# Performance work log

Hardware: AMD Instinct MI355X
Metric: run time of the kernel (lower is better)

The kernel has to match this reference:

```python
import jax, jax.numpy as jnp
import numpy as np

B, N, C = 64, 8192, 64
C4 = C // 4
EPS_BN = 1e-5


def setup_inputs() -> dict:
    key = jax.random.key(0)
    ks = jax.random.split(key, 12)
    s = 0.05
    return {
        "x": jax.random.normal(ks[0], (B, N, 10), jnp.float32),
        "y": jax.random.normal(ks[1], (B, N, 13), jnp.float32),
        "W_l": jax.random.normal(ks[2], (10, C), jnp.float32) * s,
        "b_l": jax.random.normal(ks[3], (C,), jnp.float32) * s,
        "W_r": jax.random.normal(ks[4], (13, C), jnp.float32) * s,
        "b_r": jax.random.normal(ks[5], (C,), jnp.float32) * s,
        "W_qk": jax.random.normal(ks[6], (C4, C), jnp.float32) * s,  # shared q/k 1x1-conv weight
        "W_v": jax.random.normal(ks[7], (C, C), jnp.float32) * s,
        "b_v": jax.random.normal(ks[8], (C,), jnp.float32) * s,
        "W_t": jax.random.normal(ks[9], (C, C), jnp.float32) * s,
        "b_t": jax.random.normal(ks[10], (C,), jnp.float32) * s,
        "gamma": jnp.ones((C,), jnp.float32),
        "beta": jnp.zeros((C,), jnp.float32),
    }


def reference(x, y, W_l, b_l, W_r, b_r, W_qk, W_v, b_v, W_t, b_t, gamma, beta):
    # x: [B,N,10] -> linear_l; y: [B,N,13] -> linear_r  (torch keeps [B,C,N]; we keep [B,N,C])
    X = x @ W_l + b_l                                   # [B,N,C]
    Y = y @ W_r + b_r                                   # [B,N,C]
    # 1x1 convs == per-point matmuls; attention runs ACROSS the batch dim per point n
    xq = jnp.einsum('bnc,dc->nbd', X, W_qk)             # [N,B,C/4]
    yk = jnp.einsum('bnc,dc->nbd', Y, W_qk)             # [N,B,C/4] (shared weight)
    yv = jnp.einsum('bnc,dc->nbd', Y, W_v) + b_v        # [N,B,C]
    energy = jnp.einsum('nbd,ned->nbe', xq, yk)         # [N,B,B]
    attn = jax.nn.softmax(energy, axis=-1)
    # extra L1 renormalization over dim=1 (offset-attention style)
    attn = attn / (1e-9 + attn.sum(axis=1, keepdims=True))
    yr = jnp.einsum('nbe,nec->bnc', attn, yv)           # [B,N,C]
    # trans_conv -> BatchNorm (training-mode batch stats) -> ReLU -> residual -> max over points
    t = jnp.einsum('bnc,dc->bnd', X - yr, W_t) + b_t    # [B,N,C]
    mean = t.mean(axis=(0, 1))
    var = t.var(axis=(0, 1))                            # biased var, as BN uses
    tn = gamma * (t - mean) * jax.lax.rsqrt(var + EPS_BN) + beta
    xres = X + jax.nn.relu(tn)                          # [B,N,C]
    return jnp.max(xres, axis=1)[:, :, None]            # [B,C,1] to match torch layout
```

## Files before the change

### kernel.cpp

```cpp
#include <hip/hip_runtime.h>

#define B_ 64
#define N_ 8192

using short8 = __attribute__((ext_vector_type(8))) short;
using f32x4  = __attribute__((ext_vector_type(4))) float;

#define MFMA16(a, b, c) __builtin_amdgcn_mfma_f32_16x16x32_bf16((a), (b), (c), 0, 0, 0)

__device__ inline unsigned short f2bf(float f) {
  union { float f; unsigned int u; } v; v.f = f;
  return (unsigned short)((v.u + 0x8000u) >> 16);
}
__device__ inline float bf2f(unsigned int hi16_in_low) {
  union { unsigned int u; float f; } v; v.u = hi16_in_low << 16;
  return v.f;
}


__global__ void k0_prep(const float* __restrict__ W_l, const float* __restrict__ b_l,
                        const float* __restrict__ W_r, const float* __restrict__ b_r,
                        const float* __restrict__ W_qk, const float* __restrict__ W_v,
                        const float* __restrict__ b_v, const float* __restrict__ W_t,
                        float* __restrict__ wsf) {
  const int tid = threadIdx.x;
  unsigned short* wb   = (unsigned short*)(wsf + 66688);
  unsigned short* BM   = wb;
  unsigned short* BL   = wb + 512;
  unsigned short* BRV2 = wb + 2560;
  unsigned short* BT   = wb + 4608;
  if (blockIdx.x == 0) {
    __shared__ float Wlq[11 * 16], Wrk[14 * 16];
    for (int idx = tid; idx < 11 * 16; idx += 256) {
      int i = idx >> 4, d = idx & 15;
      const float* a = (i < 10) ? (W_l + i * 64) : b_l;
      float s = 0.f;
      for (int c = 0; c < 64; ++c) s = fmaf(a[c], W_qk[d * 64 + c], s);
      Wlq[idx] = s;
    }
    for (int idx = tid; idx < 14 * 16; idx += 256) {
      int j = idx >> 4, d = idx & 15;
      const float* a = (j < 13) ? (W_r + j * 64) : b_r;
      float s = 0.f;
      for (int c = 0; c < 64; ++c) s = fmaf(a[c], W_qk[d * 64 + c], s);
      Wrk[idx] = s;
    }
    __syncthreads();
    for (int idx = tid; idx < 512; idx += 256) {
      int j = idx >> 5, kk = idx & 31;
      unsigned short o = 0;
      if (j < 14 && kk < 11) {
        float s = 0.f;
        for (int d = 0; d < 16; ++d) s = fmaf(Wlq[kk * 16 + d], Wrk[j * 16 + d], s);
        o = f2bf(s);
      }
      BM[idx] = o;
    }
  } else if (blockIdx.x == 1) {
    for (int idx = tid; idx < 2048; idx += 256) {
      int c = idx >> 5, kk = idx & 31;
      unsigned short o = 0;
      if (kk < 13) {
        float s = 0.f;
        for (int j = 0; j < 64; ++j) s = fmaf(W_r[kk * 64 + j], W_v[c * 64 + j], s);
        o = f2bf(s);
      } else if (kk == 13) {
        float s = b_v[c];
        for (int j = 0; j < 64; ++j) s = fmaf(b_r[j], W_v[c * 64 + j], s);
        o = f2bf(s);
      }
      BRV2[idx] = o;
    }
  } else if (blockIdx.x == 2) {
    for (int idx = tid; idx < 2048; idx += 256) {
      int c = idx >> 5, kk = idx & 31;
      unsigned short o = 0;
      if (kk < 10) o = f2bf(W_l[kk * 64 + c]);
      else if (kk == 10) o = f2bf(b_l[c]);
      BL[idx] = o;
    }
    for (int i = tid; i < 1024; i += 256) wsf[i] = 0.f;
  } else {
    for (int i = tid; i < 4096; i += 256) BT[i] = f2bf(W_t[i]);
  }
}

__global__ __launch_bounds__(256, 6)
void k1_attn(const float* __restrict__ x, const float* __restrict__ y,
             const float* __restrict__ wsf, const float* __restrict__ b_t,
             float* __restrict__ stats) {
  __shared__ __align__(16) short Axy[64 * 40];
  __shared__ __align__(16) short YT[16 * 72];
  __shared__ __align__(16) short awZ[4 * 1152];
  __shared__ __align__(16) short GU[4 * 256];
  __shared__ float scr[512];

  const unsigned short* wb   = (const unsigned short*)(wsf + 66688);
  const unsigned short* BM   = wb;
  const unsigned short* BL   = wb + 512;
  const unsigned short* BRV2 = wb + 2560;
  const unsigned short* BT   = wb + 4608;
  unsigned short* tg = (unsigned short*)(wsf + 66688) + 8704;

  const int n    = blockIdx.x;
  const int tid  = threadIdx.x;
  const int w    = tid >> 6;
  const int lane = tid & 63;
  const int l15  = lane & 15;
  const int q    = lane >> 4;
  const int r0   = w * 16;
  short* const aw = awZ + w * 1152;
  short* const gu = GU + w * 256;

  {
    const int b = tid >> 2, i = tid & 3;
    const float* xp = x + ((size_t)b * N_ + n) * 10;
    const float* yp = y + ((size_t)b * N_ + n) * 13;
    short* Ar = Axy + b * 40;
    Ar[i]     = (short)f2bf(xp[i]);
    Ar[i + 4] = (short)f2bf(xp[i + 4]);
    short v8 = 0;
    if (i < 2) v8 = (short)f2bf(xp[i + 8]);
    else if (i == 2) v8 = (short)0x3F80;
    Ar[i + 8]  = v8;
    Ar[i + 12] = 0;
    const short y0 = (short)f2bf(yp[i]);
    const short y1 = (short)f2bf(yp[i + 4]);
    const short y2 = (short)f2bf(yp[i + 8]);
    short y3 = 0;
    if (i == 0) y3 = (short)f2bf(yp[12]);
    else if (i == 1) y3 = (short)0x3F80;
    Ar[16 + i] = y0;  Ar[20 + i] = y1;  Ar[24 + i] = y2;  Ar[28 + i] = y3;
    YT[i * 72 + b] = y0;  YT[(i + 4) * 72 + b] = y1;
    YT[(i + 8) * 72 + b] = y2;  YT[(i + 12) * 72 + b] = y3;
  }
  __syncthreads();

  const short8 z8 = {0, 0, 0, 0, 0, 0, 0, 0};
  const f32x4 zero4 = {0.f, 0.f, 0.f, 0.f};
  const short8 aA = *(const short8*)&Axy[(r0 + l15) * 40 + q * 8];

  f32x4 G = MFMA16(aA, *(const short8*)&BM[l15 * 32 + q * 8], zero4);
  f32x4 X[4];
#pragma unroll
  for (int f = 0; f < 4; ++f)
    X[f] = MFMA16(aA, *(const short8*)&BL[(f * 16 + l15) * 32 + q * 8], zero4);
#pragma unroll
  for (int j = 0; j < 4; ++j) gu[(q * 4 + j) * 16 + l15] = (short)f2bf(G[j]);

  short8 aG = z8;
  if (q < 2) aG = *(const short8*)&gu[l15 * 16 + q * 8];
  f32x4 E[4];
#pragma unroll
  for (int f = 0; f < 4; ++f) {
    short8 bk = z8;
    if (q < 2) bk = *(const short8*)&Axy[(f * 16 + l15) * 40 + 16 + q * 8];
    E[f] = MFMA16(aG, bk, zero4);
  }

  float inv_r[4];
#pragma unroll
  for (int j = 0; j < 4; ++j) {
    float s = 0.f;
#pragma unroll
    for (int f = 0; f < 4; ++f) { E[f][j] = __expf(E[f][j]); s += E[f][j]; }
    s += __shfl_xor(s, 1);
    s += __shfl_xor(s, 2);
    s += __shfl_xor(s, 4);
    s += __shfl_xor(s, 8);
    inv_r[j] = 1.0f / s;
  }
#pragma unroll
  for (int f = 0; f < 4; ++f) {
    float cs = E[f][0] * inv_r[0] + E[f][1] * inv_r[1] + E[f][2] * inv_r[2] + E[f][3] * inv_r[3];
    cs += __shfl_xor(cs, 16);
    cs += __shfl_xor(cs, 32);
    if (lane < 16) scr[w * 64 + f * 16 + l15] = cs;
  }
  __syncthreads();
  float csvv[4];
#pragma unroll
  for (int f = 0; f < 4; ++f) {
    const int col = f * 16 + l15;
    csvv[f] = 1.0f / (1e-9f + scr[col] + scr[64 + col] + scr[128 + col] + scr[192 + col]);
  }
#pragma unroll
  for (int f = 0; f < 4; ++f)
#pragma unroll
    for (int j = 0; j < 4; ++j)
      aw[(q * 4 + j) * 72 + f * 16 + l15] = (short)f2bf(E[f][j] * inv_r[j] * csvv[f]);

  const short8 aA0 = *(const short8*)&aw[l15 * 72 + q * 8];
  const short8 aA1 = *(const short8*)&aw[l15 * 72 + 32 + q * 8];

  f32x4 U = MFMA16(aA0, *(const short8*)&YT[l15 * 72 + q * 8], zero4);
  U = MFMA16(aA1, *(const short8*)&YT[l15 * 72 + 32 + q * 8], U);
#pragma unroll
  for (int j = 0; j < 4; ++j) gu[(q * 4 + j) * 16 + l15] = (short)f2bf(U[j]);
  short8 aU = z8;
  if (q < 2) aU = *(const short8*)&gu[l15 * 16 + q * 8];

#pragma unroll
  for (int f = 0; f < 4; ++f) {
    f32x4 yr = MFMA16(aU, *(const short8*)&BRV2[(f * 16 + l15) * 32 + q * 8], zero4);
#pragma unroll
    for (int j = 0; j < 4; ++j)
      aw[(q * 4 + j) * 72 + f * 16 + l15] = (short)f2bf(X[f][j] - yr[j]);
  }

  const short8 aZ0 = *(const short8*)&aw[l15 * 72 + q * 8];
  const short8 aZ1 = *(const short8*)&aw[l15 * 72 + 32 + q * 8];
  f32x4 t[4];
#pragma unroll
  for (int f = 0; f < 4; ++f) {
    const int c = f * 16 + l15;
    const float bT = b_t[c];
    t[f] = MFMA16(aZ0, *(const short8*)&BT[c * 64 + q * 8], ((f32x4){bT, bT, bT, bT}));
    t[f] = MFMA16(aZ1, *(const short8*)&BT[c * 64 + 32 + q * 8], t[f]);
#pragma unroll
    for (int j = 0; j < 4; ++j)
      tg[(size_t)(r0 + q * 4 + j) * (N_ * 64) + (size_t)n * 64 + c] = f2bf(t[f][j]);
  }
  __syncthreads();
#pragma unroll
  for (int f = 0; f < 4; ++f) {
    float s = 0.f, ss = 0.f;
#pragma unroll
    for (int j = 0; j < 4; ++j) { s += t[f][j]; ss = fmaf(t[f][j], t[f][j], ss); }
    s  += __shfl_xor(s, 16);  s  += __shfl_xor(s, 32);
    ss += __shfl_xor(ss, 16); ss += __shfl_xor(ss, 32);
    if (lane < 16) {
      scr[w * 64 + f * 16 + l15]       = s;
      scr[256 + w * 64 + f * 16 + l15] = ss;
    }
  }
  __syncthreads();
  if (tid < 64) {
    const float s  = scr[tid] + scr[64 + tid] + scr[128 + tid] + scr[192 + tid];
    const float ss = scr[256 + tid] + scr[320 + tid] + scr[384 + tid] + scr[448 + tid];
    float* st = stats + (n & 7) * 128;
    atomicAdd(&st[tid], s);
    atomicAdd(&st[64 + tid], ss);
  }
}

__global__ void k2_stats(const float* __restrict__ stats, float* __restrict__ meanr) {
  const int c = threadIdx.x;
  if (c < 64) {
    float s = 0.f, ss = 0.f;
    for (int r = 0; r < 8; ++r) { s += stats[r * 128 + c]; ss += stats[r * 128 + 64 + c]; }
    const float inv = 1.0f / (float)(B_ * N_);
    const float mu = s * inv;
    const float var = fmaf(ss, inv, -mu * mu);
    meanr[c] = mu;
    meanr[64 + c] = rsqrtf(var + 1e-5f);
  }
}

__global__ __launch_bounds__(256)
void k3_max(const float* __restrict__ x, const float* __restrict__ W_l,
            const float* __restrict__ b_l, const float* __restrict__ gamma,
            const float* __restrict__ beta, const unsigned short* __restrict__ tg,
            const float* __restrict__ meanr, float* __restrict__ pmax)
{
  const int b = blockIdx.x >> 4;
  const int chunk = blockIdx.x & 15;
  const int wv = threadIdx.x >> 6;
  const int lane = threadIdx.x & 63;
  const int c0 = (lane & 15) * 4;
  const int nsub = lane >> 4;
  float4 wl4[10];
#pragma unroll
  for (int k = 0; k < 10; ++k) wl4[k] = *(const float4*)&W_l[k * 64 + c0];
  const float4 bl  = *(const float4*)&b_l[c0];
  const float4 g   = *(const float4*)&gamma[c0];
  const float4 be  = *(const float4*)&beta[c0];
  const float4 mu  = *(const float4*)&meanr[c0];
  const float4 rs  = *(const float4*)&meanr[64 + c0];
  float4 grs, bmb;
  grs.x = g.x * rs.x; grs.y = g.y * rs.y; grs.z = g.z * rs.z; grs.w = g.w * rs.w;
  bmb.x = be.x - mu.x * grs.x; bmb.y = be.y - mu.y * grs.y;
  bmb.z = be.z - mu.z * grs.z; bmb.w = be.w - mu.w * grs.w;
  float4 m = {-1e30f, -1e30f, -1e30f, -1e30f};
  const size_t tgb = (size_t)b << 19;
  const int n0 = chunk * 512 + wv * 128 + nsub;
  for (int jj = 0; jj < 32; ++jj) {
    const int n = n0 + jj * 4;
    const uint2 tv = *(const uint2*)&tg[tgb + (size_t)n * 64 + c0];
    const float* xp = x + ((size_t)b * N_ + n) * 10;
    float4 X = bl;
#pragma unroll
    for (int k = 0; k < 10; ++k) {
      const float xk = xp[k];
      X.x = fmaf(xk, wl4[k].x, X.x); X.y = fmaf(xk, wl4[k].y, X.y);
      X.z = fmaf(xk, wl4[k].z, X.z); X.w = fmaf(xk, wl4[k].w, X.w);
    }
    const float t0 = bf2f(tv.x & 0xFFFFu), t1 = bf2f(tv.x >> 16);
    const float t2 = bf2f(tv.y & 0xFFFFu), t3 = bf2f(tv.y >> 16);
    m.x = fmaxf(m.x, X.x + fmaxf(fmaf(t0, grs.x, bmb.x), 0.f));
    m.y = fmaxf(m.y, X.y + fmaxf(fmaf(t1, grs.y, bmb.y), 0.f));
    m.z = fmaxf(m.z, X.z + fmaxf(fmaf(t2, grs.z, bmb.z), 0.f));
    m.w = fmaxf(m.w, X.w + fmaxf(fmaf(t3, grs.w, bmb.w), 0.f));
  }
  m.x = fmaxf(m.x, __shfl_xor(m.x, 16)); m.y = fmaxf(m.y, __shfl_xor(m.y, 16));
  m.z = fmaxf(m.z, __shfl_xor(m.z, 16)); m.w = fmaxf(m.w, __shfl_xor(m.w, 16));
  m.x = fmaxf(m.x, __shfl_xor(m.x, 32)); m.y = fmaxf(m.y, __shfl_xor(m.y, 32));
  m.z = fmaxf(m.z, __shfl_xor(m.z, 32)); m.w = fmaxf(m.w, __shfl_xor(m.w, 32));
  __shared__ float sm[4][64];
  if (lane < 16) *(float4*)&sm[wv][c0] = m;
  __syncthreads();
  if (threadIdx.x < 64) {
    const float r = fmaxf(fmaxf(sm[0][threadIdx.x], sm[1][threadIdx.x]),
                          fmaxf(sm[2][threadIdx.x], sm[3][threadIdx.x]));
    pmax[(size_t)blockIdx.x * 64 + threadIdx.x] = r;
  }
}

__global__ void k4_final(const float* __restrict__ pmax, float* __restrict__ out) {
  const int b = blockIdx.x, c = threadIdx.x;
  float m = -1e30f;
  for (int ch = 0; ch < 16; ++ch) m = fmaxf(m, pmax[((size_t)b * 16 + ch) * 64 + c]);
  out[b * 64 + c] = m;
}

extern "C" void kernel_launch(void* const* d_in, const int* in_sizes, int n_in,
                              void* d_out, int out_size, void* d_ws, size_t ws_size,
                              hipStream_t stream) {
  const float* x     = (const float*)d_in[0];
  const float* y     = (const float*)d_in[1];
  const float* W_l   = (const float*)d_in[2];
  const float* b_l   = (const float*)d_in[3];
  const float* W_r   = (const float*)d_in[4];
  const float* b_r   = (const float*)d_in[5];
  const float* W_qk  = (const float*)d_in[6];
  const float* W_v   = (const float*)d_in[7];
  const float* b_v   = (const float*)d_in[8];
  const float* W_t   = (const float*)d_in[9];
  const float* b_t   = (const float*)d_in[10];
  const float* gamma = (const float*)d_in[11];
  const float* beta  = (const float*)d_in[12];
  float* out = (float*)d_out;

  float* wsf = (float*)d_ws;
  float* stats = wsf;
  float* meanr = wsf + 1024;
  float* pmax  = wsf + 1152;
  const unsigned short* tg = (const unsigned short*)(wsf + 66688) + 8704;

  hipLaunchKernelGGL(k0_prep, dim3(4), dim3(256), 0, stream,
                     W_l, b_l, W_r, b_r, W_qk, W_v, b_v, W_t, wsf);
  hipLaunchKernelGGL(k1_attn, dim3(N_), dim3(256), 0, stream,
                     x, y, wsf, b_t, stats);
  hipLaunchKernelGGL(k2_stats, dim3(1), dim3(64), 0, stream, stats, meanr);
  hipLaunchKernelGGL(k3_max, dim3(1024), dim3(256), 0, stream,
                     x, W_l, b_l, gamma, beta, tg, meanr, pmax);
  hipLaunchKernelGGL(k4_final, dim3(64), dim3(64), 0, stream, pmax, out);
}
```

Measured before the change: 208.6 us.

## Process two points per block in attention kernel to amortize weight loads and syncs

The attention kernel now handles two adjacent points per workgroup, halving the grid. The weight fragments for BM, BL and BRV2 are loaded into registers once and reused for both points, and the barrier and scratch reductions are shared across the pair. The tg global stores move to the end, after the stats atomics. In exchange the kernel uses more registers and LDS (launch bounds drop from 6 to 3 waves) and there are fewer blocks to hide latency.

New measurement: 207.2 us. Within noise of the previous version (-0.6%).

```diff
diff --git a/kernel.cpp b/kernel.cpp
--- a/kernel.cpp
+++ b/kernel.cpp
@@ -85,15 +85,16 @@
   }
 }
 
-__global__ __launch_bounds__(256, 6)
+__global__ __launch_bounds__(256, 3)
 void k1_attn(const float* __restrict__ x, const float* __restrict__ y,
              const float* __restrict__ wsf, const float* __restrict__ b_t,
              float* __restrict__ stats) {
-  __shared__ __align__(16) short Axy[64 * 40];
-  __shared__ __align__(16) short YT[16 * 72];
-  __shared__ __align__(16) short awZ[4 * 1152];
-  __shared__ __align__(16) short GU[4 * 256];
-  __shared__ float scr[512];
+  __shared__ __align__(16) short lds[18688];
+  __shared__ float scr[1024];
+  short* const Axy[2] = {lds, lds + 2560};
+  short* const YTb[2] = {lds + 5120, lds + 6272};
+  short* const awB    = lds + 7424;
+  short* const guB    = lds + 16640;
 
   const unsigned short* wb   = (const unsigned short*)(wsf + 66688);
   const unsigned short* BM   = wb;
@@ -102,146 +103,184 @@
   const unsigned short* BT   = wb + 4608;
   unsigned short* tg = (unsigned short*)(wsf + 66688) + 8704;
 
-  const int n    = blockIdx.x;
   const int tid  = threadIdx.x;
   const int w    = tid >> 6;
   const int lane = tid & 63;
   const int l15  = lane & 15;
   const int q    = lane >> 4;
   const int r0   = w * 16;
-  short* const aw = awZ + w * 1152;
-  short* const gu = GU + w * 256;
+  const int n0   = blockIdx.x * 2;
+  short* const aw[2] = {awB + w * 1152, awB + (4 + w) * 1152};
+  short* const gu[2] = {guB + w * 256,  guB + (4 + w) * 256};
 
   {
     const int b = tid >> 2, i = tid & 3;
-    const float* xp = x + ((size_t)b * N_ + n) * 10;
-    const float* yp = y + ((size_t)b * N_ + n) * 13;
-    short* Ar = Axy + b * 40;
-    Ar[i]     = (short)f2bf(xp[i]);
-    Ar[i + 4] = (short)f2bf(xp[i + 4]);
-    short v8 = 0;
-    if (i < 2) v8 = (short)f2bf(xp[i + 8]);
-    else if (i == 2) v8 = (short)0x3F80;
-    Ar[i + 8]  = v8;
-    Ar[i + 12] = 0;
-    const short y0 = (short)f2bf(yp[i]);
-    const short y1 = (short)f2bf(yp[i + 4]);
-    const short y2 = (short)f2bf(yp[i + 8]);
-    short y3 = 0;
-    if (i == 0) y3 = (short)f2bf(yp[12]);
-    else if (i == 1) y3 = (short)0x3F80;
-    Ar[16 + i] = y0;  Ar[20 + i] = y1;  Ar[24 + i] = y2;  Ar[28 + i] = y3;
-    YT[i * 72 + b] = y0;  YT[(i + 4) * 72 + b] = y1;
-    YT[(i + 8) * 72 + b] = y2;  YT[(i + 12) * 72 + b] = y3;
+#pragma unroll
+    for (int p = 0; p < 2; ++p) {
+      const float* xp = x + ((size_t)b * N_ + n0 + p) * 10;
+      const float* yp = y + ((size_t)b * N_ + n0 + p) * 13;
+      short* Ar = Axy[p] + b * 40;
+      Ar[i]     = (short)f2bf(xp[i]);
+      Ar[i + 4] = (short)f2bf(xp[i + 4]);
+      short v8 = 0;
+      if (i < 2) v8 = (short)f2bf(xp[i + 8]);
+      else if (i == 2) v8 = (short)0x3F80;
+      Ar[i + 8]  = v8;
+      Ar[i + 12] = 0;
+      const short y0 = (short)f2bf(yp[i]);
+      const short y1 = (short)f2bf(yp[i + 4]);
+      const short y2 = (short)f2bf(yp[i + 8]);
+      short y3 = 0;
+      if (i == 0) y3 = (short)f2bf(yp[12]);
+      else if (i == 1) y3 = (short)0x3F80;
+      Ar[16 + i] = y0;  Ar[20 + i] = y1;  Ar[24 + i] = y2;  Ar[28 + i] = y3;
+      short* YT = YTb[p];
+      YT[i * 72 + b] = y0;  YT[(i + 4) * 72 + b] = y1;
+      YT[(i + 8) * 72 + b] = y2;  YT[(i + 12) * 72 + b] = y3;
+    }
   }
   __syncthreads();
 
   const short8 z8 = {0, 0, 0, 0, 0, 0, 0, 0};
   const f32x4 zero4 = {0.f, 0.f, 0.f, 0.f};
-  const short8 aA = *(const short8*)&Axy[(r0 + l15) * 40 + q * 8];
-
-  f32x4 G = MFMA16(aA, *(const short8*)&BM[l15 * 32 + q * 8], zero4);
-  f32x4 X[4];
-#pragma unroll
-  for (int f = 0; f < 4; ++f)
-    X[f] = MFMA16(aA, *(const short8*)&BL[(f * 16 + l15) * 32 + q * 8], zero4);
-#pragma unroll
-  for (int j = 0; j < 4; ++j) gu[(q * 4 + j) * 16 + l15] = (short)f2bf(G[j]);
-
-  short8 aG = z8;
-  if (q < 2) aG = *(const short8*)&gu[l15 * 16 + q * 8];
-  f32x4 E[4];
-#pragma unroll
-  for (int f = 0; f < 4; ++f) {
-    short8 bk = z8;
-    if (q < 2) bk = *(const short8*)&Axy[(f * 16 + l15) * 40 + 16 + q * 8];
-    E[f] = MFMA16(aG, bk, zero4);
-  }
-
-  float inv_r[4];
-#pragma unroll
-  for (int j = 0; j < 4; ++j) {
-    float s = 0.f;
-#pragma unroll
-    for (int f = 0; f < 4; ++f) { E[f][j] = __expf(E[f][j]); s += E[f][j]; }
-    s += __shfl_xor(s, 1);
-    s += __shfl_xor(s, 2);
-    s += __shfl_xor(s, 4);
-    s += __shfl_xor(s, 8);
-    inv_r[j] = 1.0f / s;
-  }
-#pragma unroll
-  for (int f = 0; f < 4; ++f) {
-    float cs = E[f][0] * inv_r[0] + E[f][1] * inv_r[1] + E[f][2] * inv_r[2] + E[f][3] * inv_r[3];
-    cs += __shfl_xor(cs, 16);
-    cs += __shfl_xor(cs, 32);
-    if (lane < 16) scr[w * 64 + f * 16 + l15] = cs;
-  }
-  __syncthreads();
-  float csvv[4];
-#pragma unroll
-  for (int f = 0; f < 4; ++f) {
-    const int col = f * 16 + l15;
-    csvv[f] = 1.0f / (1e-9f + scr[col] + scr[64 + col] + scr[128 + col] + scr[192 + col]);
-  }
-#pragma unroll
-  for (int f = 0; f < 4; ++f)
-#pragma unroll
-    for (int j = 0; j < 4; ++j)
-      aw[(q * 4 + j) * 72 + f * 16 + l15] = (short)f2bf(E[f][j] * inv_r[j] * csvv[f]);
-
-  const short8 aA0 = *(const short8*)&aw[l15 * 72 + q * 8];
-  const short8 aA1 = *(const short8*)&aw[l15 * 72 + 32 + q * 8];
-
-  f32x4 U = MFMA16(aA0, *(const short8*)&YT[l15 * 72 + q * 8], zero4);
-  U = MFMA16(aA1, *(const short8*)&YT[l15 * 72 + 32 + q * 8], U);
-#pragma unroll
-  for (int j = 0; j < 4; ++j) gu[(q * 4 + j) * 16 + l15] = (short)f2bf(U[j]);
-  short8 aU = z8;
-  if (q < 2) aU = *(const short8*)&gu[l15 * 16 + q * 8];
-
-#pragma unroll
-  for (int f = 0; f < 4; ++f) {
-    f32x4 yr = MFMA16(aU, *(const short8*)&BRV2[(f * 16 + l15) * 32 + q * 8], zero4);
-#pragma unroll
-    for (int j = 0; j < 4; ++j)
-      aw[(q * 4 + j) * 72 + f * 16 + l15] = (short)f2bf(X[f][j] - yr[j]);
-  }
-
-  const short8 aZ0 = *(const short8*)&aw[l15 * 72 + q * 8];
-  const short8 aZ1 = *(const short8*)&aw[l15 * 72 + 32 + q * 8];
-  f32x4 t[4];
-#pragma unroll
-  for (int f = 0; f < 4; ++f) {
-    const int c = f * 16 + l15;
-    const float bT = b_t[c];
-    t[f] = MFMA16(aZ0, *(const short8*)&BT[c * 64 + q * 8], ((f32x4){bT, bT, bT, bT}));
-    t[f] = MFMA16(aZ1, *(const short8*)&BT[c * 64 + 32 + q * 8], t[f]);
-#pragma unroll
-    for (int j = 0; j < 4; ++j)
-      tg[(size_t)(r0 + q * 4 + j) * (N_ * 64) + (size_t)n * 64 + c] = f2bf(t[f][j]);
-  }
-  __syncthreads();
-#pragma unroll
-  for (int f = 0; f < 4; ++f) {
-    float s = 0.f, ss = 0.f;
-#pragma unroll
-    for (int j = 0; j < 4; ++j) { s += t[f][j]; ss = fmaf(t[f][j], t[f][j], ss); }
-    s  += __shfl_xor(s, 16);  s  += __shfl_xor(s, 32);
-    ss += __shfl_xor(ss, 16); ss += __shfl_xor(ss, 32);
-    if (lane < 16) {
-      scr[w * 64 + f * 16 + l15]       = s;
-      scr[256 + w * 64 + f * 16 + l15] = ss;
-    }
-  }
-  __syncthreads();
-  if (tid < 64) {
-    const float s  = scr[tid] + scr[64 + tid] + scr[128 + tid] + scr[192 + tid];
-    const float ss = scr[256 + tid] + scr[320 + tid] + scr[384 + tid] + scr[448 + tid];
-    float* st = stats + (n & 7) * 128;
-    atomicAdd(&st[tid], s);
-    atomicAdd(&st[64 + tid], ss);
-  }
+
+  const short8 bmF = *(const short8*)&BM[l15 * 32 + q * 8];
+  short8 blF[4];
+#pragma unroll
+  for (int f = 0; f < 4; ++f) blF[f] = *(const short8*)&BL[(f * 16 + l15) * 32 + q * 8];
+
+  f32x4 X[2][4];
+#pragma unroll
+  for (int p = 0; p < 2; ++p) {
+    const short8 aA = *(const short8*)&Axy[p][(r0 + l15) * 40 + q * 8];
+    f32x4 G = MFMA16(aA, bmF, zero4);
+#pragma unroll
+    for (int f = 0; f < 4; ++f) X[p][f] = MFMA16(aA, blF[f], zero4);
+#pragma unroll
+    for (int j = 0; j < 4; ++j) gu[p][(q * 4 + j) * 16 + l15] = (short)f2bf(G[j]);
+  }
+
+  f32x4 E[2][4];
+#pragma unroll
+  for (int p = 0; p < 2; ++p) {
+    short8 aG = z8;
+    if (q < 2) aG = *(const short8*)&gu[p][l15 * 16 + q * 8];
+#pragma unroll
+    for (int f = 0; f < 4; ++f) {
+      short8 bk = z8;
+      if (q < 2) bk = *(const short8*)&Axy[p][(f * 16 + l15) * 40 + 16 + q * 8];
+      E[p][f] = MFMA16(aG, bk, zero4);
+    }
+  }
+
+  float inv_r[2][4];
+#pragma unroll
+  for (int p = 0; p < 2; ++p)
+#pragma unroll
+    for (int j = 0; j < 4; ++j) {
+      float s = 0.f;
+#pragma unroll
+      for (int f = 0; f < 4; ++f) { E[p][f][j] = __expf(E[p][f][j]); s += E[p][f][j]; }
+      s += __shfl_xor(s, 1);
+      s += __shfl_xor(s, 2);
+      s += __shfl_xor(s, 4);
+      s += __shfl_xor(s, 8);
+      inv_r[p][j] = 1.0f / s;
+    }
+#pragma unroll
+  for (int p = 0; p < 2; ++p)
+#pragma unroll
+    for (int f = 0; f < 4; ++f) {
+      float cs = E[p][f][0] * inv_r[p][0] + E[p][f][1] * inv_r[p][1] +
+                 E[p][f][2] * inv_r[p][2] + E[p][f][3] * inv_r[p][3];
+      cs += __shfl_xor(cs, 16);
+      cs += __shfl_xor(cs, 32);
+      if (lane < 16) scr[p * 256 + w * 64 + f * 16 + l15] = cs;
+    }
+  __syncthreads();
+
+#pragma unroll
+  for (int p = 0; p < 2; ++p) {
+#pragma unroll
+    for (int f = 0; f < 4; ++f) {
+      const int col = f * 16 + l15;
+      const float* sp = scr + p * 256;
+      const float csv = 1.0f / (1e-9f + sp[col] + sp[64 + col] + sp[128 + col] + sp[192 + col]);
+#pragma unroll
+      for (int j = 0; j < 4; ++j)
+        aw[p][(q * 4 + j) * 72 + col] = (short)f2bf(E[p][f][j] * inv_r[p][j] * csv);
+    }
+  }
+
+  short8 brvF[4];
+#pragma unroll
+  for (int f = 0; f < 4; ++f) brvF[f] = *(const short8*)&BRV2[(f * 16 + l15) * 32 + q * 8];
+#pragma unroll
+  for (int p = 0; p < 2; ++p) {
+    const short8 aA0 = *(const short8*)&aw[p][l15 * 72 + q * 8];
+    const short8 aA1 = *(const short8*)&aw[p][l15 * 72 + 32 + q * 8];
+    f32x4 U = MFMA16(aA0, *(const short8*)&YTb[p][l15 * 72 + q * 8], zero4);
+    U = MFMA16(aA1, *(const short8*)&YTb[p][l15 * 72 + 32 + q * 8], U);
+#pragma unroll
+    for (int j = 0; j < 4; ++j) gu[p][(q * 4 + j) * 16 + l15] = (short)f2bf(U[j]);
+    short8 aU = z8;
+    if (q < 2) aU = *(const short8*)&gu[p][l15 * 16 + q * 8];
+#pragma unroll
+    for (int f = 0; f < 4; ++f) {
+      f32x4 yr = MFMA16(aU, brvF[f], zero4);
+#pragma unroll
+      for (int j = 0; j < 4; ++j)
+        aw[p][(q * 4 + j) * 72 + f * 16 + l15] = (short)f2bf(X[p][f][j] - yr[j]);
+    }
+  }
+
+  f32x4 t[2][4];
+  float sRed[2][4], ssRed[2][4];
+#pragma unroll
+  for (int p = 0; p < 2; ++p) {
+    const short8 aZ0 = *(const short8*)&aw[p][l15 * 72 + q * 8];
+    const short8 aZ1 = *(const short8*)&aw[p][l15 * 72 + 32 + q * 8];
+#pragma unroll
+    for (int f = 0; f < 4; ++f) {
+      const int c = f * 16 + l15;
+      const float bT = b_t[c];
+      t[p][f] = MFMA16(aZ0, *(const short8*)&BT[c * 64 + q * 8], ((f32x4){bT, bT, bT, bT}));
+      t[p][f] = MFMA16(aZ1, *(const short8*)&BT[c * 64 + 32 + q * 8], t[p][f]);
+      float s = 0.f, ss = 0.f;
+#pragma unroll
+      for (int j = 0; j < 4; ++j) { s += t[p][f][j]; ss = fmaf(t[p][f][j], t[p][f][j], ss); }
+      s  += __shfl_xor(s, 16);  s  += __shfl_xor(s, 32);
+      ss += __shfl_xor(ss, 16); ss += __shfl_xor(ss, 32);
+      sRed[p][f] = s; ssRed[p][f] = ss;
+    }
+  }
+  __syncthreads();
+#pragma unroll
+  for (int p = 0; p < 2; ++p)
+#pragma unroll
+    for (int f = 0; f < 4; ++f)
+      if (lane < 16) {
+        scr[p * 512 + w * 64 + f * 16 + l15]       = sRed[p][f];
+        scr[p * 512 + 256 + w * 64 + f * 16 + l15] = ssRed[p][f];
+      }
+  __syncthreads();
+  if (tid < 128) {
+    const int p = tid >> 6, c = tid & 63;
+    const float* sp = scr + p * 512;
+    const float s  = sp[c] + sp[64 + c] + sp[128 + c] + sp[192 + c];
+    const float ss = sp[256 + c] + sp[320 + c] + sp[384 + c] + sp[448 + c];
+    float* st = stats + ((n0 + p) & 7) * 128;
+    atomicAdd(&st[c], s);
+    atomicAdd(&st[64 + c], ss);
+  }
+#pragma unroll
+  for (int p = 0; p < 2; ++p)
+#pragma unroll
+    for (int f = 0; f < 4; ++f)
+#pragma unroll
+      for (int j = 0; j < 4; ++j)
+        tg[(size_t)(r0 + q * 4 + j) * (N_ * 64) + (size_t)(n0 + p) * 64 + f * 16 + l15] =
+            f2bf(t[p][f][j]);
 }
 
 __global__ void k2_stats(const float* __restrict__ stats, float* __restrict__ meanr) {
@@ -349,7 +388,7 @@
 
   hipLaunchKernelGGL(k0_prep, dim3(4), dim3(256), 0, stream,
                      W_l, b_l, W_r, b_r, W_qk, W_v, b_v, W_t, wsf);
-  hipLaunchKernelGGL(k1_attn, dim3(N_), dim3(256), 0, stream,
+  hipLaunchKernelGGL(k1_attn, dim3(N_ / 2), dim3(256), 0, stream,
                      x, y, wsf, b_t, stats);
   hipLaunchKernelGGL(k2_stats, dim3(1), dim3(64), 0, stream, stats, meanr);
   hipLaunchKernelGGL(k3_max, dim3(1024), dim3(256), 0, stream,
```
